# Performance work log

Hardware: AMD Instinct MI355X
Metric: run time of the kernel (lower is better)

The kernel has to match this reference:

```python
import jax, jax.numpy as jnp
import numpy as np

EMBEDDING_LENGTH = 2048
EMBEDDING_DIM = 4


def setup_inputs() -> dict:
    key = jax.random.key(0)
    kx, ke = jax.random.split(key)
    x = jax.random.uniform(kx, (16, 64, 64, EMBEDDING_DIM), dtype=jnp.float32)
    embedding = jax.random.uniform(ke, (EMBEDDING_LENGTH, EMBEDDING_DIM), dtype=jnp.float32)
    return {"x": x, "embedding": embedding}


def reference(x, embedding):
    # x: [B, w, h, c], embedding: [K, c]
    B, w, h, c = x.shape
    flat = x.reshape(-1, c)  # [N, c], N = B*w*h
    # ||f - e||^2 = ||f||^2 - 2 f.e + ||e||^2 (avoids materializing [N, K, c])
    x2 = jnp.sum(flat * flat, axis=-1, keepdims=True)          # [N, 1]
    e2 = jnp.sum(embedding * embedding, axis=-1)               # [K]
    dots = jnp.einsum('nc,kc->nk', flat, embedding)            # [N, K]
    dists = x2 - 2.0 * dots + e2                               # [N, K]
    idx = jnp.argmin(dists, axis=-1)                           # [N] int
    return idx.reshape(B, w, h)
```

## Files before the change

### kernel.cpp

```cpp
#include <hip/hip_runtime.h>
#include <math.h>

#pragma clang fp contract(off)

typedef __attribute__((ext_vector_type(2))) float f2;

constexpr int KCODES = 2048;
constexpr int CDIM   = 4;
constexpr int KSPLIT = 8;
constexpr int KCHUNK = KCODES / KSPLIT;
constexpr int RPT    = 2;
constexpr int ROWSPB = 64 * RPT;
constexpr int NUNITS = KCODES / 2;

__device__ __forceinline__ float min3f(float a, float b, float c) {
    float d; asm("v_min3_f32 %0, %1, %2, %3" : "=v"(d) : "v"(a), "v"(b), "v"(c)); return d;
}
__device__ __forceinline__ float sumsq(float4 e) {
    return ((e.x * e.x + e.y * e.y) + e.z * e.z) + e.w * e.w;
}

__global__ __launch_bounds__(512) void vq_fused(
    const float* __restrict__ x,
    const float* __restrict__ emb,
    int* __restrict__ out,
    int N)
{
    __shared__ float4 sEP[NUNITS * 2];
    __shared__ float4 sSP[KCODES / 4];

    const float4* __restrict__ embf4 = reinterpret_cast<const float4*>(emb);
    const int t = threadIdx.x;

    for (int j = t; j < NUNITS; j += 512) {
        float4 a = embf4[2 * j], b = embf4[2 * j + 1];
        sEP[2 * j]     = make_float4(a.x, b.x, a.y, b.y);
        sEP[2 * j + 1] = make_float4(a.z, b.z, a.w, b.w);
    }
    for (int q = t; q < KCODES / 4; q += 512) {
        float4 e0 = embf4[4 * q],     e1 = embf4[4 * q + 1];
        float4 e2 = embf4[4 * q + 2], e3 = embf4[4 * q + 3];
        sSP[q] = make_float4(sumsq(e0), sumsq(e1), sumsq(e2), sumsq(e3));
    }
    __syncthreads();

    const int lane = t & 63;
    const int wid   = __builtin_amdgcn_readfirstlane(t >> 6);
    const int kbase = wid * KCHUNK;
    const int ubase = kbase >> 1;
    const int qbase = kbase >> 2;
    const int nbase = blockIdx.x * ROWSPB + lane;

    float4 xv[RPT];
    f2 xx[RPT], yy[RPT], zz[RPT], ww[RPT], x2p[RPT];
    float dmin[RPT];
    int   bu[RPT];
    #pragma unroll
    for (int r = 0; r < RPT; ++r) {
        const int n = nbase + r * 64;
        xv[r] = (n < N) ? reinterpret_cast<const float4*>(x)[n]
                        : make_float4(0.f, 0.f, 0.f, 0.f);
        const float x2 = ((xv[r].x * xv[r].x + xv[r].y * xv[r].y)
                          + xv[r].z * xv[r].z) + xv[r].w * xv[r].w;
        xx[r] = f2{xv[r].x, xv[r].x}; yy[r] = f2{xv[r].y, xv[r].y};
        zz[r] = f2{xv[r].z, xv[r].z}; ww[r] = f2{xv[r].w, xv[r].w};
        x2p[r] = f2{x2, x2};
        dmin[r] = HUGE_VALF; bu[r] = ubase;
    }
    const f2 m2 = {-2.0f, -2.0f};

    for (int g = 0; g < KCHUNK / 8; ++g) {
        const float4 sA = sSP[qbase + 2 * g];
        const float4 sB = sSP[qbase + 2 * g + 1];
        const int u0 = ubase + 4 * g;
        #pragma unroll
        for (int uu = 0; uu < 4; ++uu) {
            const float4 qa = sEP[2 * (u0 + uu)];
            const float4 qb = sEP[2 * (u0 + uu) + 1];
            const f2 ea = {qa.x, qa.y}, eb = {qa.z, qa.w};
            const f2 ec = {qb.x, qb.y}, ed = {qb.z, qb.w};
            const f2 sp = (uu == 0) ? f2{sA.x, sA.y} :
                          (uu == 1) ? f2{sA.z, sA.w} :
                          (uu == 2) ? f2{sB.x, sB.y} : f2{sB.z, sB.w};
            #pragma unroll
            for (int r = 0; r < RPT; ++r) {
                f2 dot = xx[r] * ea;
                dot = __builtin_elementwise_fma(yy[r], eb, dot);
                dot = __builtin_elementwise_fma(zz[r], ec, dot);
                dot = __builtin_elementwise_fma(ww[r], ed, dot);
                f2 dd = __builtin_elementwise_fma(m2, dot, x2p[r]) + sp;
                float nd = min3f(dmin[r], dd.x, dd.y);
                bu[r] = (nd < dmin[r]) ? (u0 + uu) : bu[r];
                dmin[r] = nd;
            }
        }
    }

    const float2* __restrict__ sSPf2 = reinterpret_cast<const float2*>(sSP);
    unsigned long long key[RPT];
    #pragma unroll
    for (int r = 0; r < RPT; ++r) {
        const int u = bu[r];
        const float4 qa = sEP[2 * u];
        const float4 qb = sEP[2 * u + 1];
        const float2 sv = sSPf2[u];
        float dot = xv[r].x * qa.x;
        dot = __builtin_fmaf(xv[r].y, qa.z, dot);
        dot = __builtin_fmaf(xv[r].z, qb.x, dot);
        dot = __builtin_fmaf(xv[r].w, qb.z, dot);
        const float de = __builtin_fmaf(-2.0f, dot, x2p[r].x) + sv.x;
        const int idx = 2 * u + ((de == dmin[r]) ? 0 : 1);
        key[r] = ((unsigned long long)__float_as_uint(dmin[r]) << 32)
                 | (unsigned)idx;
    }

    __syncthreads();
    unsigned long long* skey = reinterpret_cast<unsigned long long*>(sEP);
    #pragma unroll
    for (int r = 0; r < RPT; ++r)
        skey[(r * 64 + lane) * (KSPLIT + 1) + wid] = key[r];
    __syncthreads();

    if (t < ROWSPB) {
        const int rn = blockIdx.x * ROWSPB + t;
        if (rn < N) {
            unsigned long long k = skey[t * (KSPLIT + 1)];
            #pragma unroll
            for (int s = 1; s < KSPLIT; ++s) {
                unsigned long long v = skey[t * (KSPLIT + 1) + s];
                if (v < k) k = v;
            }
            out[rn] = (int)(unsigned)(k & 0xFFFFFFFFull);
        }
    }
}

extern "C" void kernel_launch(void* const* d_in, const int* in_sizes, int n_in,
                              void* d_out, int out_size, void* d_ws, size_t ws_size,
                              hipStream_t stream) {
    const float* x   = (const float*)d_in[0];
    const float* emb = (const float*)d_in[1];
    int* out = (int*)d_out;
    const int N = in_sizes[0] / CDIM;

    vq_fused<<<(N + ROWSPB - 1) / ROWSPB, 512, 0, stream>>>(x, emb, out, N);
}
```

Baseline: 28.29 us.

## Pre-scale codebook by -2 and track best group of eight codes with scalar FMAs

The codebook is stored in shared memory already multiplied by -2, so each distance is x2 + dot + e2 with no separate -2 multiply. The inner loop drops packed float2 math and runs scalar FMAs over eight codes per group, reducing them with four min3 ops. It keeps only the winning group index and recomputes the eight candidates afterward to recover the exact code index. Launch bounds now request four waves per SIMD. The trade is more scalar FMA instructions than the packed version against fewer select and min operations per code, plus an epilogue that reloads eight codes.

Result: no change. 28.17 us (-0.4%).

```diff
diff --git a/kernel.cpp b/kernel.cpp
--- a/kernel.cpp
+++ b/kernel.cpp
@@ -2,8 +2,6 @@
 #include <math.h>
 
 #pragma clang fp contract(off)
-
-typedef __attribute__((ext_vector_type(2))) float f2;
 
 constexpr int KCODES = 2048;
 constexpr int CDIM   = 4;
@@ -11,7 +9,6 @@
 constexpr int KCHUNK = KCODES / KSPLIT;
 constexpr int RPT    = 2;
 constexpr int ROWSPB = 64 * RPT;
-constexpr int NUNITS = KCODES / 2;
 
 __device__ __forceinline__ float min3f(float a, float b, float c) {
     float d; asm("v_min3_f32 %0, %1, %2, %3" : "=v"(d) : "v"(a), "v"(b), "v"(c)); return d;
@@ -20,102 +17,118 @@
     return ((e.x * e.x + e.y * e.y) + e.z * e.z) + e.w * e.w;
 }
 
-__global__ __launch_bounds__(512) void vq_fused(
+__global__ __launch_bounds__(512, 4) void vq_fused(
     const float* __restrict__ x,
     const float* __restrict__ emb,
     int* __restrict__ out,
     int N)
 {
-    __shared__ float4 sEP[NUNITS * 2];
-    __shared__ float4 sSP[KCODES / 4];
+    __shared__ float4 sE[KCODES];
+    __shared__ float4 sS[KCODES / 4];
 
     const float4* __restrict__ embf4 = reinterpret_cast<const float4*>(emb);
     const int t = threadIdx.x;
 
-    for (int j = t; j < NUNITS; j += 512) {
-        float4 a = embf4[2 * j], b = embf4[2 * j + 1];
-        sEP[2 * j]     = make_float4(a.x, b.x, a.y, b.y);
-        sEP[2 * j + 1] = make_float4(a.z, b.z, a.w, b.w);
+    for (int i = t; i < KCODES; i += 512) {
+        float4 e = embf4[i];
+        sE[i] = make_float4(-2.0f * e.x, -2.0f * e.y, -2.0f * e.z, -2.0f * e.w);
     }
     for (int q = t; q < KCODES / 4; q += 512) {
         float4 e0 = embf4[4 * q],     e1 = embf4[4 * q + 1];
         float4 e2 = embf4[4 * q + 2], e3 = embf4[4 * q + 3];
-        sSP[q] = make_float4(sumsq(e0), sumsq(e1), sumsq(e2), sumsq(e3));
+        sS[q] = make_float4(sumsq(e0), sumsq(e1), sumsq(e2), sumsq(e3));
     }
     __syncthreads();
 
     const int lane = t & 63;
     const int wid   = __builtin_amdgcn_readfirstlane(t >> 6);
     const int kbase = wid * KCHUNK;
-    const int ubase = kbase >> 1;
     const int qbase = kbase >> 2;
     const int nbase = blockIdx.x * ROWSPB + lane;
 
-    float4 xv[RPT];
-    f2 xx[RPT], yy[RPT], zz[RPT], ww[RPT], x2p[RPT];
+    float x0[RPT], x1[RPT], x2c[RPT], x3[RPT], xs[RPT];
     float dmin[RPT];
-    int   bu[RPT];
+    int   bg[RPT];
     #pragma unroll
     for (int r = 0; r < RPT; ++r) {
         const int n = nbase + r * 64;
-        xv[r] = (n < N) ? reinterpret_cast<const float4*>(x)[n]
-                        : make_float4(0.f, 0.f, 0.f, 0.f);
-        const float x2 = ((xv[r].x * xv[r].x + xv[r].y * xv[r].y)
-                          + xv[r].z * xv[r].z) + xv[r].w * xv[r].w;
-        xx[r] = f2{xv[r].x, xv[r].x}; yy[r] = f2{xv[r].y, xv[r].y};
-        zz[r] = f2{xv[r].z, xv[r].z}; ww[r] = f2{xv[r].w, xv[r].w};
-        x2p[r] = f2{x2, x2};
-        dmin[r] = HUGE_VALF; bu[r] = ubase;
+        float4 xv = (n < N) ? reinterpret_cast<const float4*>(x)[n]
+                            : make_float4(0.f, 0.f, 0.f, 0.f);
+        x0[r] = xv.x; x1[r] = xv.y; x2c[r] = xv.z; x3[r] = xv.w;
+        xs[r] = ((xv.x * xv.x + xv.y * xv.y) + xv.z * xv.z) + xv.w * xv.w;
+        dmin[r] = HUGE_VALF; bg[r] = 0;
     }
-    const f2 m2 = {-2.0f, -2.0f};
 
+    #pragma unroll 2
     for (int g = 0; g < KCHUNK / 8; ++g) {
-        const float4 sA = sSP[qbase + 2 * g];
-        const float4 sB = sSP[qbase + 2 * g + 1];
-        const int u0 = ubase + 4 * g;
+        const int k0 = kbase + (g << 3);
+        const float4 e0 = sE[k0 + 0], e1 = sE[k0 + 1];
+        const float4 e2 = sE[k0 + 2], e3 = sE[k0 + 3];
+        const float4 e4 = sE[k0 + 4], e5 = sE[k0 + 5];
+        const float4 e6 = sE[k0 + 6], e7 = sE[k0 + 7];
+        const float4 sA = sS[qbase + 2 * g];
+        const float4 sB = sS[qbase + 2 * g + 1];
+
         #pragma unroll
-        for (int uu = 0; uu < 4; ++uu) {
-            const float4 qa = sEP[2 * (u0 + uu)];
-            const float4 qb = sEP[2 * (u0 + uu) + 1];
-            const f2 ea = {qa.x, qa.y}, eb = {qa.z, qa.w};
-            const f2 ec = {qb.x, qb.y}, ed = {qb.z, qb.w};
-            const f2 sp = (uu == 0) ? f2{sA.x, sA.y} :
-                          (uu == 1) ? f2{sA.z, sA.w} :
-                          (uu == 2) ? f2{sB.x, sB.y} : f2{sB.z, sB.w};
-            #pragma unroll
-            for (int r = 0; r < RPT; ++r) {
-                f2 dot = xx[r] * ea;
-                dot = __builtin_elementwise_fma(yy[r], eb, dot);
-                dot = __builtin_elementwise_fma(zz[r], ec, dot);
-                dot = __builtin_elementwise_fma(ww[r], ed, dot);
-                f2 dd = __builtin_elementwise_fma(m2, dot, x2p[r]) + sp;
-                float nd = min3f(dmin[r], dd.x, dd.y);
-                bu[r] = (nd < dmin[r]) ? (u0 + uu) : bu[r];
-                dmin[r] = nd;
-            }
+        for (int r = 0; r < RPT; ++r) {
+            const float a0 = x0[r], a1 = x1[r], a2 = x2c[r], a3 = x3[r];
+            const float xq = xs[r];
+            const float prev = dmin[r];
+
+            #define VQ_D(EV, SV, OUTV)                                   \
+                do {                                                     \
+                    float dt = a0 * EV.x;                                \
+                    dt = __builtin_fmaf(a1, EV.y, dt);                   \
+                    dt = __builtin_fmaf(a2, EV.z, dt);                   \
+                    dt = __builtin_fmaf(a3, EV.w, dt);                   \
+                    OUTV = (xq + dt) + SV;                               \
+                } while (0)
+
+            float d0, d1, d2, d3, d4, d5, d6, d7;
+            VQ_D(e0, sA.x, d0); VQ_D(e1, sA.y, d1);
+            VQ_D(e2, sA.z, d2); VQ_D(e3, sA.w, d3);
+            VQ_D(e4, sB.x, d4); VQ_D(e5, sB.y, d5);
+            VQ_D(e6, sB.z, d6); VQ_D(e7, sB.w, d7);
+            #undef VQ_D
+
+            float m = min3f(dmin[r], d0, d1);
+            m = min3f(m, d2, d3);
+            m = min3f(m, d4, d5);
+            m = min3f(m, d6, d7);
+            bg[r] = (m < prev) ? g : bg[r];
+            dmin[r] = m;
         }
     }
 
-    const float2* __restrict__ sSPf2 = reinterpret_cast<const float2*>(sSP);
     unsigned long long key[RPT];
     #pragma unroll
     for (int r = 0; r < RPT; ++r) {
-        const int u = bu[r];
-        const float4 qa = sEP[2 * u];
-        const float4 qb = sEP[2 * u + 1];
-        const float2 sv = sSPf2[u];
-        float dot = xv[r].x * qa.x;
-        dot = __builtin_fmaf(xv[r].y, qa.z, dot);
-        dot = __builtin_fmaf(xv[r].z, qb.x, dot);
-        dot = __builtin_fmaf(xv[r].w, qb.z, dot);
-        const float de = __builtin_fmaf(-2.0f, dot, x2p[r].x) + sv.x;
-        const int idx = 2 * u + ((de == dmin[r]) ? 0 : 1);
+        const int k0 = kbase + (bg[r] << 3);
+        const float a0 = x0[r], a1 = x1[r], a2 = x2c[r], a3 = x3[r];
+        const float xq = xs[r];
+        int idx = 0x7fffffff;
+        #pragma unroll
+        for (int h = 0; h < 2; ++h) {
+            const float4 sv = sS[(k0 >> 2) + h];
+            const float ss[4] = {sv.x, sv.y, sv.z, sv.w};
+            #pragma unroll
+            for (int j = 0; j < 4; ++j) {
+                const int k = k0 + 4 * h + j;
+                const float4 e = sE[k];
+                float dt = a0 * e.x;
+                dt = __builtin_fmaf(a1, e.y, dt);
+                dt = __builtin_fmaf(a2, e.z, dt);
+                dt = __builtin_fmaf(a3, e.w, dt);
+                const float d = (xq + dt) + ss[j];
+                idx = min(idx, (d == dmin[r]) ? k : 0x7fffffff);
+            }
+        }
         key[r] = ((unsigned long long)__float_as_uint(dmin[r]) << 32)
                  | (unsigned)idx;
     }
 
     __syncthreads();
-    unsigned long long* skey = reinterpret_cast<unsigned long long*>(sEP);
+    unsigned long long* skey = reinterpret_cast<unsigned long long*>(sE);
     #pragma unroll
     for (int r = 0; r < RPT; ++r)
         skey[(r * 64 + lane) * (KSPLIT + 1) + wid] = key[r];
```
